# Kernel optimization log

Measured on AMD Instinct MI355X. Metric: run time of the kernel, lower is better.

## Reference

```python
import jax, jax.numpy as jnp
import numpy as np

D_MODEL = 1024
N_HEADS = 16
HEAD_DIM = D_MODEL // N_HEADS


def setup_inputs() -> dict:
    key = jax.random.key(0)
    k_x, k_wqkv, k_bqkv, k_wp, k_bp = jax.random.split(key, 5)
    B, S = 4, 2048
    bound_qkv = 1.0 / np.sqrt(D_MODEL)
    bound_p = 1.0 / np.sqrt(D_MODEL)
    return {
        "x": jax.random.normal(k_x, (B, S, D_MODEL), dtype=jnp.float32),
        # torch nn.Linear weight is [out, in]; store transposed [in, out] for x @ W
        "w_qkv": jax.random.uniform(k_wqkv, (D_MODEL, 3 * D_MODEL), minval=-bound_qkv, maxval=bound_qkv, dtype=jnp.float32),
        "b_qkv": jax.random.uniform(k_bqkv, (3 * D_MODEL,), minval=-bound_qkv, maxval=bound_qkv, dtype=jnp.float32),
        "w_proj": jax.random.uniform(k_wp, (D_MODEL, D_MODEL), minval=-bound_p, maxval=bound_p, dtype=jnp.float32),
        "b_proj": jax.random.uniform(k_bp, (D_MODEL,), minval=-bound_p, maxval=bound_p, dtype=jnp.float32),
    }


def reference(x, w_qkv, b_qkv, w_proj, b_proj):
    B, S, C = x.shape
    qkv = x @ w_qkv + b_qkv  # [B, S, 3C]
    q, k, v = jnp.split(qkv, 3, axis=-1)
    # [B, H, S, Dh]
    q = q.reshape(B, S, N_HEADS, HEAD_DIM).transpose(0, 2, 1, 3)
    k = k.reshape(B, S, N_HEADS, HEAD_DIM).transpose(0, 2, 1, 3)
    v = v.reshape(B, S, N_HEADS, HEAD_DIM).transpose(0, 2, 1, 3)
    scale = 1.0 / np.sqrt(HEAD_DIM).astype(np.float32)
    att = jnp.einsum("bhqd,bhkd->bhqk", q, k) * scale  # [B, H, S, S]
    causal = jnp.tril(jnp.ones((S, S), dtype=bool))
    att = jnp.where(causal[None, None], att, -jnp.inf)
    att = jax.nn.softmax(att, axis=-1)
    # dropout p=0.0 -> identity
    y = jnp.einsum("bhqk,bhkd->bhqd", att, v)  # [B, H, S, Dh]
    y = y.transpose(0, 2, 1, 3).reshape(B, S, C)
    return y @ w_proj + b_proj
```

## Files before the change

### kernel.cpp

```cpp
#include <hip/hip_runtime.h>
#include <stdint.h>

typedef __attribute__((ext_vector_type(8))) short bf8_t;
typedef __attribute__((ext_vector_type(4))) short bf4_t;
typedef __attribute__((ext_vector_type(4))) float f4_t;

#define D_MODEL 1024
#define SEQ 2048
#define NB 4
#define NH 16
#define HD 64
#define MROWS (NB * SEQ)
#define QSCALE 0.1803368801111204f

__device__ __forceinline__ uint16_t f2bf(float f) {
  uint32_t u = __builtin_bit_cast(uint32_t, f);
  u += 0x7FFFu + ((u >> 16) & 1u);
  return (uint16_t)(u >> 16);
}

__device__ __forceinline__ void gload16(const void* g, void* l) {
  __builtin_amdgcn_global_load_lds(
      (const __attribute__((address_space(1))) void*)g,
      (__attribute__((address_space(3))) void*)l, 16, 0, 0);
}

__global__ void k_cvt(const float* __restrict__ in, uint16_t* __restrict__ out, int n4) {
  int i = blockIdx.x * blockDim.x + threadIdx.x;
  if (i >= n4) return;
  float4 v = ((const float4*)in)[i];
  ushort4 o;
  o.x = f2bf(v.x); o.y = f2bf(v.y); o.z = f2bf(v.z); o.w = f2bf(v.w);
  ((ushort4*)out)[i] = o;
}

__global__ void k_tcvt(const float* __restrict__ in, uint16_t* __restrict__ out, int K, int N) {
  __shared__ float tile[32][33];
  int nb = blockIdx.x * 32, kb = blockIdx.y * 32;
  int tx = threadIdx.x & 31, ty = threadIdx.x >> 5;
#pragma unroll
  for (int i = 0; i < 4; ++i)
    tile[ty + i * 8][tx] = in[(size_t)(kb + ty + i * 8) * N + nb + tx];
  __syncthreads();
#pragma unroll
  for (int i = 0; i < 4; ++i)
    out[(size_t)(nb + ty + i * 8) * K + kb + tx] = f2bf(tile[tx][ty + i * 8]);
}

template <int MREP, int NWN, int BROWS>
__device__ __forceinline__ void mainloop8(const uint16_t* __restrict__ A,
                                          const uint16_t* __restrict__ Bt,
                                          int mBase, int nBase,
                                          uint16_t* __restrict__ AsB,
                                          uint16_t* __restrict__ BsB,
                                          f4_t (&acc)[MREP][4]) {
  constexpr int BLOADS = BROWS / 64;
  const int t = threadIdx.x, lane = t & 63;
  const int g = lane >> 4, a = lane & 15;
  const int wave = t >> 6, wm = wave / NWN, wn = wave % NWN;
  const int sr = t >> 3;
  const int sc = (t & 7) ^ (sr & 7);
  const uint16_t* Ag[4];
  const uint16_t* Bg[BLOADS];
#pragma unroll
  for (int l = 0; l < 4; ++l)
    Ag[l] = A + (size_t)(mBase + l * 64 + sr) * D_MODEL + sc * 8;
#pragma unroll
  for (int l = 0; l < BLOADS; ++l)
    Bg[l] = Bt + (size_t)(nBase + l * 64 + sr) * D_MODEL + sc * 8;

  auto stage = [&](int kt, int buf) {
#pragma unroll
    for (int l = 0; l < 4; ++l)
      gload16(Ag[l] + kt * 64, AsB + buf * (256 * 64) + (l * 512 + t) * 8);
#pragma unroll
    for (int l = 0; l < BLOADS; ++l)
      gload16(Bg[l] + kt * 64, BsB + buf * (BROWS * 64) + (l * 512 + t) * 8);
  };

  stage(0, 0);
  for (int kt = 0; kt < D_MODEL / 64; ++kt) {
    const int buf = kt & 1;
    if (kt < D_MODEL / 64 - 1) {
      stage(kt + 1, buf ^ 1);
      if constexpr (BLOADS == 4) asm volatile("s_waitcnt vmcnt(8)" ::: "memory");
      else                       asm volatile("s_waitcnt vmcnt(6)" ::: "memory");
    } else {
      asm volatile("s_waitcnt vmcnt(0)" ::: "memory");
    }
    __builtin_amdgcn_s_barrier();
    __builtin_amdgcn_sched_barrier(0);
    const char* Ab = (const char*)(AsB + buf * (256 * 64));
    const char* Bb = (const char*)(BsB + buf * (BROWS * 64));
    bf8_t bfr[4][2];
#pragma unroll
    for (int ni = 0; ni < 4; ++ni) {
      int row = wn * 64 + ni * 16 + a;
#pragma unroll
      for (int kk = 0; kk < 2; ++kk)
        bfr[ni][kk] = *(const bf8_t*)(Bb + row * 128 + (((4 * kk + g) ^ (row & 7)) * 16));
    }
#pragma unroll
    for (int s = 0; s < MREP / 2; ++s) {
      bf8_t af[2][2];
#pragma unroll
      for (int mm = 0; mm < 2; ++mm) {
        int row = wm * (MREP * 16) + (2 * s + mm) * 16 + a;
#pragma unroll
        for (int kk = 0; kk < 2; ++kk)
          af[mm][kk] = *(const bf8_t*)(Ab + row * 128 + (((4 * kk + g) ^ (row & 7)) * 16));
      }
      __builtin_amdgcn_s_setprio(1);
#pragma unroll
      for (int mm = 0; mm < 2; ++mm)
#pragma unroll
        for (int ni = 0; ni < 4; ++ni) {
          acc[2 * s + mm][ni] = __builtin_amdgcn_mfma_f32_16x16x32_bf16(af[mm][0], bfr[ni][0], acc[2 * s + mm][ni], 0, 0, 0);
          acc[2 * s + mm][ni] = __builtin_amdgcn_mfma_f32_16x16x32_bf16(af[mm][1], bfr[ni][1], acc[2 * s + mm][ni], 0, 0, 0);
        }
      __builtin_amdgcn_s_setprio(0);
    }
    asm volatile("s_waitcnt lgkmcnt(0)" ::: "memory");
    __builtin_amdgcn_s_barrier();
    __builtin_amdgcn_sched_barrier(0);
  }
}

__global__ __launch_bounds__(512, 2) void k_gemm_qkv(
    const uint16_t* __restrict__ A, const uint16_t* __restrict__ Bt,
    const float* __restrict__ bias,
    uint16_t* __restrict__ Qb, uint16_t* __restrict__ Kb, uint16_t* __restrict__ VTb) {
  __shared__ uint16_t As[2][256 * 64];
  __shared__ uint16_t Bs[2][256 * 64];
  int flat = blockIdx.x;
  int swz = (flat & 7) * 48 + (flat >> 3);
  int bx = swz % 12, by = swz / 12;
  int mBase = by * 256, nBase = bx * 256;
  f4_t acc[8][4] = {};
  mainloop8<8, 4, 256>(A, Bt, mBase, nBase, &As[0][0], &Bs[0][0], acc);
  const int lane = threadIdx.x & 63, g = lane >> 4, a = lane & 15;
  const int wave = threadIdx.x >> 6, wm = wave >> 2, wn = wave & 3;
  float bi[4];
#pragma unroll
  for (int ni = 0; ni < 4; ++ni) bi[ni] = bias[nBase + wn * 64 + ni * 16 + a];
#pragma unroll
  for (int mi = 0; mi < 8; ++mi)
#pragma unroll
    for (int ni = 0; ni < 4; ++ni)
#pragma unroll
      for (int i = 0; i < 4; ++i) {
        int m = mBase + wm * 128 + mi * 16 + 4 * g + i;
        int n = nBase + wn * 64 + ni * 16 + a;
        float v = acc[mi][ni][i] + bi[ni];
        int b = m >> 11, s = m & 2047;
        int which = n >> 10, hn = n & 1023;
        int h = hn >> 6, d = hn & 63;
        size_t bh = (size_t)(b * NH + h);
        if (which == 0)      Qb[(bh * SEQ + s) * HD + d] = f2bf(v * QSCALE);
        else if (which == 1) Kb[(bh * SEQ + s) * HD + d] = f2bf(v);
        else                 VTb[(bh * HD + d) * SEQ + s] = f2bf(v);
      }
}

__global__ __launch_bounds__(512, 2) void k_gemm_proj(
    const uint16_t* __restrict__ A, const uint16_t* __restrict__ Bt,
    const float* __restrict__ bias, float* __restrict__ out) {
  __shared__ uint16_t As[2][256 * 64];
  __shared__ uint16_t Bs[2][128 * 64];
  int flat = blockIdx.x;
  int swz = (flat & 7) * 32 + (flat >> 3);
  int bx = swz % 8, by = swz / 8;
  int mBase = by * 256, nBase = bx * 128;
  f4_t acc[4][4] = {};
  mainloop8<4, 2, 128>(A, Bt, mBase, nBase, &As[0][0], &Bs[0][0], acc);
  const int lane = threadIdx.x & 63, g = lane >> 4, a = lane & 15;
  const int wave = threadIdx.x >> 6, wm = wave >> 1, wn = wave & 1;
  float bi[4];
#pragma unroll
  for (int ni = 0; ni < 4; ++ni) bi[ni] = bias[nBase + wn * 64 + ni * 16 + a];
#pragma unroll
  for (int mi = 0; mi < 4; ++mi)
#pragma unroll
    for (int ni = 0; ni < 4; ++ni)
#pragma unroll
      for (int i = 0; i < 4; ++i) {
        int m = mBase + wm * 64 + mi * 16 + 4 * g + i;
        int n = nBase + wn * 64 + ni * 16 + a;
        out[(size_t)m * D_MODEL + n] = acc[mi][ni][i] + bi[ni];
      }
}

__global__ __launch_bounds__(512, 4) void k_attn(
    const uint16_t* __restrict__ Qb, const uint16_t* __restrict__ Kb,
    const uint16_t* __restrict__ VTb, uint16_t* __restrict__ Yb) {
  __shared__ uint16_t Ks[2][64 * 64];
  __shared__ uint16_t Vs[2][64 * 64];
  const int t = threadIdx.x, lane = t & 63, wave = t >> 6;
  const int g = lane >> 4, a = lane & 15;
  const int bh = blockIdx.x, pr = blockIdx.y;
  const int b = bh >> 4, h = bh & 15;

  const int sr = t >> 3;
  const int scol = (t & 7) ^ (sr & 7);
  const uint16_t* Kg = Kb + ((size_t)bh * SEQ + sr) * HD + scol * 8;
  const uint16_t* Vg = VTb + ((size_t)bh * HD + sr) * SEQ + scol * 8;

#pragma unroll 1
  for (int seg = 0; seg < 2; ++seg) {
    const int qt = seg ? (15 - pr) : pr;
    const int qrow0 = qt * 128 + wave * 16;
    const uint16_t* Qrow = Qb + ((size_t)bh * SEQ + qrow0 + a) * HD;
    bf8_t aq[2];
    aq[0] = *(const bf8_t*)(Qrow + g * 8);
    aq[1] = *(const bf8_t*)(Qrow + g * 8 + 32);
    float m_i = -__builtin_inff(), l_i = 0.f;
    f4_t O[4] = {};

    const int nt = 2 * qt + 2;
    gload16(Kg, Ks[0] + t * 8);
    gload16(Vg, Vs[0] + t * 8);

    for (int kt = 0; kt < nt; ++kt) {
      const int cur = kt & 1;
      if (kt + 1 < nt) {
        gload16(Kg + (size_t)(kt + 1) * 64 * HD, Ks[cur ^ 1] + t * 8);
        gload16(Vg + (kt + 1) * 64, Vs[cur ^ 1] + t * 8);
        asm volatile("s_waitcnt vmcnt(2)" ::: "memory");
      } else {
        asm volatile("s_waitcnt vmcnt(0)" ::: "memory");
      }
      __builtin_amdgcn_s_barrier();

      const uint16_t* Kt = Ks[cur];
      const uint16_t* Vt = Vs[cur];
      if (kt * 64 <= qrow0 + 15) {
        f4_t sacc[4] = {};
#pragma unroll
        for (int f = 0; f < 4; ++f) {
          int kr = f * 16 + a;
#pragma unroll
          for (int kx = 0; kx < 2; ++kx) {
            int gl = g + kx * 4;
            bf8_t bk = *(const bf8_t*)((const char*)Kt + kr * 128 + ((gl ^ (kr & 7)) * 16));
            sacc[f] = __builtin_amdgcn_mfma_f32_16x16x32_bf16(bk, aq[kx], sacc[f], 0, 0, 0);
          }
        }
        if (kt >= 2 * qt) {
          int q = qrow0 + a;
#pragma unroll
          for (int f = 0; f < 4; ++f)
#pragma unroll
            for (int i = 0; i < 4; ++i) {
              int key = kt * 64 + f * 16 + g * 4 + i;
              if (key > q) sacc[f][i] = -__builtin_inff();
            }
        }
        float mx = sacc[0][0];
#pragma unroll
        for (int f = 0; f < 4; ++f)
#pragma unroll
          for (int i = 0; i < 4; ++i) mx = fmaxf(mx, sacc[f][i]);
        mx = fmaxf(mx, __shfl_xor(mx, 16));
        mx = fmaxf(mx, __shfl_xor(mx, 32));
        if (__any(mx > m_i + 8.0f)) {
          float mN = fmaxf(m_i, mx);
          float sc2 = exp2f(m_i - mN);
          m_i = mN;
          l_i *= sc2;
#pragma unroll
          for (int i = 0; i < 4; ++i) {
            float s4 = __shfl(sc2, (lane & 48) | (g * 4 + i));
#pragma unroll
            for (int f2 = 0; f2 < 4; ++f2) O[f2][i] *= s4;
          }
        }
        float pvv[4][4];
        float sm = 0.f;
#pragma unroll
        for (int f = 0; f < 4; ++f)
#pragma unroll
          for (int i = 0; i < 4; ++i) {
            pvv[f][i] = exp2f(sacc[f][i] - m_i);
            sm += pvv[f][i];
          }
        sm += __shfl_xor(sm, 16);
        sm += __shfl_xor(sm, 32);
        l_i += sm;
        bf8_t pa[2];
#pragma unroll
        for (int kx = 0; kx < 2; ++kx)
#pragma unroll
          for (int j = 0; j < 8; ++j)
            pa[kx][j] = (short)f2bf(pvv[2 * kx + (j >> 2)][j & 3]);
#pragma unroll
        for (int kx = 0; kx < 2; ++kx)
#pragma unroll
          for (int f2 = 0; f2 < 4; ++f2) {
            int rv = f2 * 16 + a;
            int sw = (rv & 7) << 4;
            bf4_t lo = *(const bf4_t*)((const char*)Vt + rv * 128 + ((64 * kx + 8 * g) ^ sw));
            bf4_t hi = *(const bf4_t*)((const char*)Vt + rv * 128 + ((64 * kx + 32 + 8 * g) ^ sw));
            bf8_t bv = __builtin_shufflevector(lo, hi, 0, 1, 2, 3, 4, 5, 6, 7);
            O[f2] = __builtin_amdgcn_mfma_f32_16x16x32_bf16(pa[kx], bv, O[f2], 0, 0, 0);
          }
      }
      asm volatile("s_waitcnt lgkmcnt(0)" ::: "memory");
      __builtin_amdgcn_s_barrier();
    }
    float rinv[4];
#pragma unroll
    for (int i = 0; i < 4; ++i)
      rinv[i] = 1.0f / __shfl(l_i, (lane & 48) | (g * 4 + i));
#pragma unroll
    for (int f2 = 0; f2 < 4; ++f2)
#pragma unroll
      for (int i = 0; i < 4; ++i) {
        int q = qrow0 + g * 4 + i;
        int d = f2 * 16 + a;
        Yb[((size_t)b * SEQ + q) * D_MODEL + h * HD + d] = f2bf(O[f2][i] * rinv[i]);
      }
  }
}

extern "C" void kernel_launch(void* const* d_in, const int* in_sizes, int n_in,
                              void* d_out, int out_size, void* d_ws, size_t ws_size,
                              hipStream_t stream) {
  const float* x     = (const float*)d_in[0];
  const float* wqkv  = (const float*)d_in[1];
  const float* bqkv  = (const float*)d_in[2];
  const float* wproj = (const float*)d_in[3];
  const float* bproj = (const float*)d_in[4];
  float* out = (float*)d_out;
  char* ws = (char*)d_ws;
  uint16_t* xb     = (uint16_t*)(ws);
  uint16_t* wqkvT  = (uint16_t*)(ws + 16777216);
  uint16_t* wprojT = (uint16_t*)(ws + 16777216 + 6291456);
  uint16_t* Qb     = (uint16_t*)(ws + 25165824);
  uint16_t* Kb     = (uint16_t*)(ws + 25165824 + 16777216);
  uint16_t* VTb    = (uint16_t*)(ws + 25165824 + 2 * 16777216);
  uint16_t* Yb     = (uint16_t*)(ws + 25165824 + 3 * 16777216);

  k_cvt<<<dim3(MROWS * D_MODEL / 4 / 256), dim3(256), 0, stream>>>(x, xb, MROWS * D_MODEL / 4);
  k_tcvt<<<dim3(3 * D_MODEL / 32, D_MODEL / 32), dim3(256), 0, stream>>>(wqkv, wqkvT, D_MODEL, 3 * D_MODEL);
  k_tcvt<<<dim3(D_MODEL / 32, D_MODEL / 32), dim3(256), 0, stream>>>(wproj, wprojT, D_MODEL, D_MODEL);
  k_gemm_qkv<<<dim3(384), dim3(512), 0, stream>>>(xb, wqkvT, bqkv, Qb, Kb, VTb);
  k_attn<<<dim3(NB * NH, 8), dim3(512), 0, stream>>>(Qb, Kb, VTb, Yb);
  k_gemm_proj<<<dim3(256), dim3(512), 0, stream>>>(Yb, wprojT, bproj, out);
}
```

Measured before the change: 303.8 us.

## Interleave GEMM global loads with MFMA phases and permute V layout for 16-byte reads

The GEMM mainloop is restructured into a finer-grained schedule. Each iteration covers two k-tiles in eight sub-phases, and each sub-phase issues a half-stage of A or B global-to-LDS loads ahead of its MFMA block, replacing one bulk prefetch per k-tile. The projection GEMM switches to a 2x4 wave layout with a 256x128 tile. The QKV epilogue also permutes V's sequence index within 64-element blocks so the attention kernel can fetch each PV operand with one 16-byte LDS read instead of two 8-byte reads plus a shuffle. The cost is more barriers per k-tile and a more fragile vmcnt accounting.

```diff
diff --git a/kernel.cpp b/kernel.cpp
--- a/kernel.cpp
+++ b/kernel.cpp
@@ -2,7 +2,6 @@
 #include <stdint.h>
 
 typedef __attribute__((ext_vector_type(8))) short bf8_t;
-typedef __attribute__((ext_vector_type(4))) short bf4_t;
 typedef __attribute__((ext_vector_type(4))) float f4_t;
 
 #define D_MODEL 1024
@@ -47,82 +46,107 @@
     out[(size_t)(nb + ty + i * 8) * K + kb + tx] = f2bf(tile[tx][ty + i * 8]);
 }
 
-template <int MREP, int NWN, int BROWS>
-__device__ __forceinline__ void mainloop8(const uint16_t* __restrict__ A,
-                                          const uint16_t* __restrict__ Bt,
-                                          int mBase, int nBase,
-                                          uint16_t* __restrict__ AsB,
-                                          uint16_t* __restrict__ BsB,
-                                          f4_t (&acc)[MREP][4]) {
-  constexpr int BLOADS = BROWS / 64;
+template <int NREP>
+__device__ __forceinline__ void mainloop8p(const uint16_t* __restrict__ A,
+                                           const uint16_t* __restrict__ Bt,
+                                           int mBase, int nBase,
+                                           uint16_t* __restrict__ AsB,
+                                           uint16_t* __restrict__ BsB,
+                                           f4_t (&acc)[8][NREP]) {
+  constexpr int AELEM = 256 * 64;
+  constexpr int BELEM = NREP * 64 * 64;
   const int t = threadIdx.x, lane = t & 63;
   const int g = lane >> 4, a = lane & 15;
-  const int wave = t >> 6, wm = wave / NWN, wn = wave % NWN;
+  const int wave = t >> 6, wm = wave >> 2, wn = wave & 3;
   const int sr = t >> 3;
   const int sc = (t & 7) ^ (sr & 7);
+
   const uint16_t* Ag[4];
-  const uint16_t* Bg[BLOADS];
 #pragma unroll
   for (int l = 0; l < 4; ++l)
     Ag[l] = A + (size_t)(mBase + l * 64 + sr) * D_MODEL + sc * 8;
-#pragma unroll
-  for (int l = 0; l < BLOADS; ++l)
+  const uint16_t* Bg[NREP];
+#pragma unroll
+  for (int l = 0; l < NREP; ++l)
     Bg[l] = Bt + (size_t)(nBase + l * 64 + sr) * D_MODEL + sc * 8;
 
-  auto stage = [&](int kt, int buf) {
-#pragma unroll
-    for (int l = 0; l < 4; ++l)
-      gload16(Ag[l] + kt * 64, AsB + buf * (256 * 64) + (l * 512 + t) * 8);
-#pragma unroll
-    for (int l = 0; l < BLOADS; ++l)
-      gload16(Bg[l] + kt * 64, BsB + buf * (BROWS * 64) + (l * 512 + t) * 8);
+  auto stageA = [&](int kt, int h) {
+    int buf = kt & 1;
+#pragma unroll
+    for (int l = h; l < 4; l += 2)
+      gload16(Ag[l] + kt * 64, AsB + buf * AELEM + (l * 512 + t) * 8);
   };
-
-  stage(0, 0);
-  for (int kt = 0; kt < D_MODEL / 64; ++kt) {
-    const int buf = kt & 1;
-    if (kt < D_MODEL / 64 - 1) {
-      stage(kt + 1, buf ^ 1);
-      if constexpr (BLOADS == 4) asm volatile("s_waitcnt vmcnt(8)" ::: "memory");
-      else                       asm volatile("s_waitcnt vmcnt(6)" ::: "memory");
-    } else {
-      asm volatile("s_waitcnt vmcnt(0)" ::: "memory");
-    }
-    __builtin_amdgcn_s_barrier();
-    __builtin_amdgcn_sched_barrier(0);
-    const char* Ab = (const char*)(AsB + buf * (256 * 64));
-    const char* Bb = (const char*)(BsB + buf * (BROWS * 64));
-    bf8_t bfr[4][2];
-#pragma unroll
-    for (int ni = 0; ni < 4; ++ni) {
-      int row = wn * 64 + ni * 16 + a;
-#pragma unroll
-      for (int kk = 0; kk < 2; ++kk)
-        bfr[ni][kk] = *(const bf8_t*)(Bb + row * 128 + (((4 * kk + g) ^ (row & 7)) * 16));
-    }
-#pragma unroll
-    for (int s = 0; s < MREP / 2; ++s) {
+  auto stageB = [&](int kt, int h) {
+    int buf = kt & 1;
+#pragma unroll
+    for (int l = h * (NREP / 2); l < (h + 1) * (NREP / 2); ++l)
+      gload16(Bg[l] + kt * 64, BsB + buf * BELEM + (l * 512 + t) * 8);
+  };
+
+  stageA(0, 0); stageA(0, 1); stageB(0, 0); stageB(0, 1);
+  stageB(1, 0); stageA(1, 0); stageB(1, 1);
+  if constexpr (NREP == 4) asm volatile("s_waitcnt vmcnt(6)" ::: "memory");
+  else                     asm volatile("s_waitcnt vmcnt(4)" ::: "memory");
+  __builtin_amdgcn_s_barrier();
+
+  bf8_t bfr[NREP][2];
+  constexpr int stA[8] = {1, 0, 1, 0, 1, 0, 1, 0};
+  constexpr int stK[8] = {1, 2, 2, 2, 2, 3, 3, 3};
+  constexpr int stH[8] = {1, 0, 0, 1, 1, 0, 0, 1};
+
+#pragma unroll 1
+  for (int it = 0; it < 8; ++it) {
+    const int ka = 2 * it;
+#pragma unroll
+    for (int p = 0; p < 8; ++p) {
+      const int s = p & 3;
+      const int buf = p >> 2;
+      const char* Ab = (const char*)(AsB + buf * AELEM);
+      const char* Bb = (const char*)(BsB + buf * BELEM);
+      if (s == 0) {
+#pragma unroll
+        for (int ni = 0; ni < NREP; ++ni) {
+          int row = wn * (NREP * 16) + ni * 16 + a;
+#pragma unroll
+          for (int kk = 0; kk < 2; ++kk)
+            bfr[ni][kk] = *(const bf8_t*)(Bb + row * 128 + (((4 * kk + g) ^ (row & 7)) * 16));
+        }
+      }
       bf8_t af[2][2];
 #pragma unroll
       for (int mm = 0; mm < 2; ++mm) {
-        int row = wm * (MREP * 16) + (2 * s + mm) * 16 + a;
+        int row = wm * 128 + (2 * s + mm) * 16 + a;
 #pragma unroll
         for (int kk = 0; kk < 2; ++kk)
           af[mm][kk] = *(const bf8_t*)(Ab + row * 128 + (((4 * kk + g) ^ (row & 7)) * 16));
       }
+      {
+        int tkt = ka + stK[p];
+        if (tkt < D_MODEL / 64) {
+          if (stA[p]) stageA(tkt, stH[p]);
+          else        stageB(tkt, stH[p]);
+        }
+      }
+      __builtin_amdgcn_s_barrier();
+      asm volatile("s_waitcnt lgkmcnt(0)" ::: "memory");
+      __builtin_amdgcn_sched_barrier(0);
       __builtin_amdgcn_s_setprio(1);
 #pragma unroll
       for (int mm = 0; mm < 2; ++mm)
 #pragma unroll
-        for (int ni = 0; ni < 4; ++ni) {
+        for (int ni = 0; ni < NREP; ++ni) {
           acc[2 * s + mm][ni] = __builtin_amdgcn_mfma_f32_16x16x32_bf16(af[mm][0], bfr[ni][0], acc[2 * s + mm][ni], 0, 0, 0);
           acc[2 * s + mm][ni] = __builtin_amdgcn_mfma_f32_16x16x32_bf16(af[mm][1], bfr[ni][1], acc[2 * s + mm][ni], 0, 0, 0);
         }
       __builtin_amdgcn_s_setprio(0);
+      if (p == 3 || p == 7) {
+        if (it == 7)             asm volatile("s_waitcnt vmcnt(0)" ::: "memory");
+        else if constexpr (NREP == 4) asm volatile("s_waitcnt vmcnt(6)" ::: "memory");
+        else                     asm volatile("s_waitcnt vmcnt(4)" ::: "memory");
+      }
+      __builtin_amdgcn_s_barrier();
+      __builtin_amdgcn_sched_barrier(0);
     }
-    asm volatile("s_waitcnt lgkmcnt(0)" ::: "memory");
-    __builtin_amdgcn_s_barrier();
-    __builtin_amdgcn_sched_barrier(0);
   }
 }
 
@@ -137,7 +161,7 @@
   int bx = swz % 12, by = swz / 12;
   int mBase = by * 256, nBase = bx * 256;
   f4_t acc[8][4] = {};
-  mainloop8<8, 4, 256>(A, Bt, mBase, nBase, &As[0][0], &Bs[0][0], acc);
+  mainloop8p<4>(A, Bt, mBase, nBase, &As[0][0], &Bs[0][0], acc);
   const int lane = threadIdx.x & 63, g = lane >> 4, a = lane & 15;
   const int wave = threadIdx.x >> 6, wm = wave >> 2, wn = wave & 3;
   float bi[4];
@@ -158,7 +182,11 @@
         size_t bh = (size_t)(b * NH + h);
         if (which == 0)      Qb[(bh * SEQ + s) * HD + d] = f2bf(v * QSCALE);
         else if (which == 1) Kb[(bh * SEQ + s) * HD + d] = f2bf(v);
-        else                 VTb[(bh * HD + d) * SEQ + s] = f2bf(v);
+        else {
+          int x = s & 63;
+          int sp = (s & ~63) | (x & 0x23) | ((x & 0x0C) << 1) | ((x & 0x10) >> 2);
+          VTb[(bh * HD + d) * SEQ + sp] = f2bf(v);
+        }
       }
 }
 
@@ -171,21 +199,21 @@
   int swz = (flat & 7) * 32 + (flat >> 3);
   int bx = swz % 8, by = swz / 8;
   int mBase = by * 256, nBase = bx * 128;
-  f4_t acc[4][4] = {};
-  mainloop8<4, 2, 128>(A, Bt, mBase, nBase, &As[0][0], &Bs[0][0], acc);
+  f4_t acc[8][2] = {};
+  mainloop8p<2>(A, Bt, mBase, nBase, &As[0][0], &Bs[0][0], acc);
   const int lane = threadIdx.x & 63, g = lane >> 4, a = lane & 15;
-  const int wave = threadIdx.x >> 6, wm = wave >> 1, wn = wave & 1;
-  float bi[4];
-#pragma unroll
-  for (int ni = 0; ni < 4; ++ni) bi[ni] = bias[nBase + wn * 64 + ni * 16 + a];
-#pragma unroll
-  for (int mi = 0; mi < 4; ++mi)
-#pragma unroll
-    for (int ni = 0; ni < 4; ++ni)
+  const int wave = threadIdx.x >> 6, wm = wave >> 2, wn = wave & 3;
+  float bi[2];
+#pragma unroll
+  for (int ni = 0; ni < 2; ++ni) bi[ni] = bias[nBase + wn * 32 + ni * 16 + a];
+#pragma unroll
+  for (int mi = 0; mi < 8; ++mi)
+#pragma unroll
+    for (int ni = 0; ni < 2; ++ni)
 #pragma unroll
       for (int i = 0; i < 4; ++i) {
-        int m = mBase + wm * 64 + mi * 16 + 4 * g + i;
-        int n = nBase + wn * 64 + ni * 16 + a;
+        int m = mBase + wm * 128 + mi * 16 + 4 * g + i;
+        int n = nBase + wn * 32 + ni * 16 + a;
         out[(size_t)m * D_MODEL + n] = acc[mi][ni][i] + bi[ni];
       }
 }
@@ -297,10 +325,7 @@
 #pragma unroll
           for (int f2 = 0; f2 < 4; ++f2) {
             int rv = f2 * 16 + a;
-            int sw = (rv & 7) << 4;
-            bf4_t lo = *(const bf4_t*)((const char*)Vt + rv * 128 + ((64 * kx + 8 * g) ^ sw));
-            bf4_t hi = *(const bf4_t*)((const char*)Vt + rv * 128 + ((64 * kx + 32 + 8 * g) ^ sw));
-            bf8_t bv = __builtin_shufflevector(lo, hi, 0, 1, 2, 3, 4, 5, 6, 7);
+            bf8_t bv = *(const bf8_t*)((const char*)Vt + rv * 128 + (((4 * kx + g) ^ (rv & 7)) * 16));
             O[f2] = __builtin_amdgcn_mfma_f32_16x16x32_bf16(pa[kx], bv, O[f2], 0, 0, 0);
           }
       }
```

Measured after the change: 295.9 us. 1.03x faster.
